# Kernel optimization log

Measured on AMD Instinct MI355X. Metric: run time of the kernel, lower is better.

The kernel has to match this reference:

```python
import jax, jax.numpy as jnp
import numpy as np

N_RAYS = 32768
HID = 64
MARCH_ITERS = 64
EPS = 1e-4
NEAR = 0.0
FAR = 1.0
T_FAR = 1.0
TPUT_B = 64
JITTER = 1.0 / TPUT_B  # fixed stand-in for random.random() * (2 / batch_size)


def _init_linear(key, fan_in, fan_out):
    kw, kb = jax.random.split(key)
    lim = 1.0 / np.sqrt(fan_in)
    W = jax.random.uniform(kw, (fan_in, fan_out), jnp.float32, -lim, lim)
    b = jax.random.uniform(kb, (fan_out,), jnp.float32, -lim, lim)
    return W, b


def setup_inputs() -> dict:
    key = jax.random.key(0)
    ks = jax.random.split(key, 6)
    rays = jax.random.normal(ks[0], (N_RAYS, 6), jnp.float32)
    W0, b0 = _init_linear(ks[1], 3, HID)
    W1, b1 = _init_linear(ks[2], HID, HID)
    W2, b2 = _init_linear(ks[3], HID, 1)
    Wr0, br0 = _init_linear(ks[4], 6, HID)
    Wr1, br1 = _init_linear(ks[5], HID, 3)
    return dict(rays=rays, W0=W0, b0=b0, W1=W1, b1=b1, W2=W2, b2=b2,
                Wr0=Wr0, br0=br0, Wr1=Wr1, br1=br1)


def _sdf(p, W0, b0, W1, b1, W2, b2):
    # p: [N, 3] -> signed distance [N, 1]
    h = jax.nn.relu(p @ W0 + b0)
    h = jax.nn.relu(h @ W1 + b1)
    return h @ W2 + b2


def _refl(p, d, Wr0, br0, Wr1, br1):
    # p, d: [N, 3] -> RGB [N, 3]
    h = jax.nn.relu(jnp.concatenate([p, d], axis=-1) @ Wr0 + br0)
    return jax.nn.sigmoid(h @ Wr1 + br1)


def reference(rays, W0, b0, W1, b1, W2, b2, Wr0, br0, Wr1, br1):
    r_o, r_d = rays[..., :3], rays[..., 3:]
    sdf = lambda p: _sdf(p, W0, b0, W1, b1, W2, b2)

    # --- sphere march (64 fixed iterations; early-exit break is a no-op
    # once all rays hit, since hit rays stop updating) ---
    hits0 = jnp.zeros(r_o.shape[:-1] + (1,), jnp.bool_)
    dist0 = jnp.full(r_o.shape[:-1] + (1,), NEAR, jnp.float32)

    def march(carry, _):
        hits, cd = carry
        d = sdf(r_o + r_d * cd)  # [N, 1]
        hits = hits | ((d < EPS) & (cd >= NEAR) & (cd <= FAR))
        cd = jnp.where(~hits, cd + d, cd)
        return (hits, cd), None

    (hit, t), _ = jax.lax.scan(march, (hits0, dist0), None, length=MARCH_ITERS)
    pts = r_o + r_d * t

    rgb = _refl(pts, r_d, Wr0, br0, Wr1, br1)
    rgb = jnp.where(hit, rgb, 0.0)  # out[~hit] = 0

    # --- throughput (index search under no_grad in the original) ---
    max_t = T_FAR + JITTER
    step = max_t / TPUT_B
    sg = jax.lax.stop_gradient
    sdf_ng = lambda p: _sdf(p, sg(W0), sg(b0), sg(W1), sg(b1), sg(W2), sg(b2))
    r_o_ng, r_d_ng = sg(r_o), sg(r_d)

    curr_min0 = sdf_ng(r_o_ng)[..., 0]          # [N]
    idxs0 = jnp.zeros_like(curr_min0, jnp.int32)

    def tloop(carry, i):
        cm, idxs = carry
        t_i = step * (i + 1).astype(jnp.float32)
        sd = sdf_ng(r_o_ng + t_i * r_d_ng)[..., 0]
        idxs = jnp.where(sd < cm, i + 1, idxs)
        return (jnp.minimum(cm, sd), idxs), None

    (_, idxs), _ = jax.lax.scan(tloop, (curr_min0, idxs0),
                                jnp.arange(TPUT_B, dtype=jnp.int32))

    best_pos = r_o + idxs[..., None].astype(jnp.float32) * step * r_d  # [N, 3]
    tput = sdf(best_pos)  # [N, 1], differentiable (outside no_grad in torch)

    return jnp.concatenate([rgb, tput], axis=-1)  # [N, 4]
```

## Files before the change

kernel.cpp:

```cpp
#include <hip/hip_runtime.h>
#include <math.h>

#define NRAYS        32768
#define MARCH_ITERS  64
#define EPS_         1e-4f
#define STEP_        ((1.0f + 1.0f/64.0f) / 64.0f)

typedef __attribute__((ext_vector_type(8)))  short    short8;
typedef __attribute__((ext_vector_type(4)))  float    float4v;
typedef __attribute__((ext_vector_type(4)))  unsigned uint4v;

__device__ __forceinline__ short8 mk_frag(unsigned p0, unsigned p1,
                                          unsigned p2, unsigned p3) {
    uint4v v = {p0, p1, p2, p3};
    return __builtin_bit_cast(short8, v);
}

__device__ __forceinline__ unsigned packbf(unsigned a, unsigned b) {
    return __builtin_amdgcn_perm(b, a, 0x07060302u);
}

struct Split3 { unsigned h, m, l; };
__device__ __forceinline__ Split3 split3(float x) {
    unsigned xu = __float_as_uint(x);
    float xh = __uint_as_float(xu & 0xFFFF0000u);
    float r  = x - xh;
    unsigned ru = __float_as_uint(r);
    float xm = __uint_as_float(ru & 0xFFFF0000u);
    float r2 = r - xm;
    return { xu, ru, __float_as_uint(r2) };
}

struct Split2 { unsigned h, r; };
__device__ __forceinline__ Split2 split2(float x) {
    unsigned xu = __float_as_uint(x);
    float xh = __uint_as_float(xu & 0xFFFF0000u);
    float rr = x - xh;
    return { xu, __float_as_uint(rr) };
}

__global__ __launch_bounds__(64)
__attribute__((amdgpu_waves_per_eu(2, 2)))
void sdf_w7_k(
    const float* __restrict__ rays,
    const float* __restrict__ W0,  const float* __restrict__ b0,
    const float* __restrict__ W1,  const float* __restrict__ b1,
    const float* __restrict__ W2,  const float* __restrict__ b2,
    const float* __restrict__ Wr0, const float* __restrict__ br0,
    const float* __restrict__ Wr1, const float* __restrict__ br1,
    float* __restrict__ out)
{
    const int lane = threadIdx.x;
    const int kind = blockIdx.x & 1;
    const int quad = lane >> 4;
    const int m    = lane & 15;
    const int rayBase = (blockIdx.x >> 1) * 16;

    const float* rp = rays + (rayBase + m) * 6;
    const float ox = rp[0], oy = rp[1], oz = rp[2];
    const float dx = rp[3], dy = rp[4], dz = rp[5];

    short8 A1[4];
    {
        const float* wbase = (quad == 0) ? W0 : (quad == 1) ? (W0 + 64)
                           : (quad == 2) ? (W0 + 128) : b0;
        #pragma unroll
        for (int t = 0; t < 4; ++t) {
            int j = 32 * (t >> 1) + 8 * (m >> 2) + 4 * (t & 1) + (m & 3);
            Split3 s = split3(wbase[j]);
            unsigned hh = packbf(s.h, s.h);
            unsigned hm = packbf(s.h, s.m);
            unsigned ml = packbf(s.m, s.l);
            unsigned l0 = packbf(s.l, 0u);
            bool is3 = (quad == 3);
            A1[t] = mk_frag(is3 ? hm : hh, is3 ? l0 : hm, is3 ? 0u : ml, 0u);
        }
    }

    float4v b1v[4], w2v[4];
    #pragma unroll
    for (int t = 0; t < 4; ++t) {
        int base = 16 * t + 4 * quad;
        b1v[t] = (float4v){b1[base], b1[base + 1], b1[base + 2], b1[base + 3]};
        w2v[t] = (float4v){W2[base], W2[base + 1], W2[base + 2], W2[base + 3]};
    }
    const float b2s = b2[0];
    const float4v z4 = {0.f, 0.f, 0.f, 0.f};

    auto buildB1 = [&](float px, float py, float pz) -> short8 {
        float c = (quad == 0) ? px : (quad == 1) ? py : pz;
        Split3 s = split3(c);
        unsigned d0 = packbf(s.h, s.m);
        unsigned d1 = packbf(s.l, s.h);
        unsigned d2 = packbf(s.m, s.h);
        if (quad == 3) { d0 = 0x3F803F80u; d1 = 0x00003F80u; d2 = 0u; }
        return mk_frag(d0, d1, d2, 0u);
    };

    auto front = [&](float px, float py, float pz, short8* BH, short8* BM) {
        short8 B1 = buildB1(px, py, pz);
        float4v C1[4];
        #pragma unroll
        for (int t = 0; t < 4; ++t)
            C1[t] = __builtin_amdgcn_mfma_f32_16x16x32_bf16(A1[t], B1, z4, 0, 0, 0);
        unsigned PH[4][2], PM[4][2];
        #pragma unroll
        for (int t = 0; t < 4; ++t) {
            float v0 = fmaxf(C1[t][0], 0.f), v1 = fmaxf(C1[t][1], 0.f);
            float v2 = fmaxf(C1[t][2], 0.f), v3 = fmaxf(C1[t][3], 0.f);
            unsigned u0 = __float_as_uint(v0), u1 = __float_as_uint(v1);
            unsigned u2 = __float_as_uint(v2), u3 = __float_as_uint(v3);
            PH[t][0] = packbf(u0, u1); PH[t][1] = packbf(u2, u3);
            float r0 = v0 - __uint_as_float(u0 & 0xFFFF0000u);
            float r1 = v1 - __uint_as_float(u1 & 0xFFFF0000u);
            float r2 = v2 - __uint_as_float(u2 & 0xFFFF0000u);
            float r3 = v3 - __uint_as_float(u3 & 0xFFFF0000u);
            PM[t][0] = packbf(__float_as_uint(r0), __float_as_uint(r1));
            PM[t][1] = packbf(__float_as_uint(r2), __float_as_uint(r3));
        }
        #pragma unroll
        for (int h = 0; h < 2; ++h) {
            BH[h] = mk_frag(PH[2 * h][0], PH[2 * h][1],
                            PH[2 * h + 1][0], PH[2 * h + 1][1]);
            BM[h] = mk_frag(PM[2 * h][0], PM[2 * h][1],
                            PM[2 * h + 1][0], PM[2 * h + 1][1]);
        }
    };

    auto l3 = [&](const float4v* C2) -> float {
        float q0 = 0.f, q1 = 0.f, q2 = 0.f, q3 = 0.f;
        #pragma unroll
        for (int t = 0; t < 4; ++t) {
            q0 = fmaf(fmaxf(C2[t][0], 0.f), w2v[t][0], q0);
            q1 = fmaf(fmaxf(C2[t][1], 0.f), w2v[t][1], q1);
            q2 = fmaf(fmaxf(C2[t][2], 0.f), w2v[t][2], q2);
            q3 = fmaf(fmaxf(C2[t][3], 0.f), w2v[t][3], q3);
        }
        float part = (q0 + q1) + (q2 + q3);
        part += __shfl_xor(part, 16, 64);
        part += __shfl_xor(part, 32, 64);
        return b2s + part;
    };

    if (kind == 0) {
        short8 A2h[2][4], A2m[2][4];
        #pragma unroll
        for (int h = 0; h < 2; ++h)
            #pragma unroll
            for (int t = 0; t < 4; ++t) {
                unsigned pm[4], ph[4];
                #pragma unroll
                for (int jp = 0; jp < 4; ++jp) {
                    int k0 = 32 * h + quad * 8 + 2 * jp;
                    int j2 = 16 * t + m;
                    Split2 a = split2(W1[k0 * 64 + j2]);
                    Split2 b = split2(W1[(k0 + 1) * 64 + j2]);
                    pm[jp] = packbf(a.r, b.r);
                    ph[jp] = packbf(a.h, b.h);
                }
                A2m[h][t] = mk_frag(pm[0], pm[1], pm[2], pm[3]);
                A2h[h][t] = mk_frag(ph[0], ph[1], ph[2], ph[3]);
            }

        bool  hit = false;
        float cd  = 0.f;
        #pragma unroll 1
        for (int it = 0; it < MARCH_ITERS; ++it) {
            if (__all(hit)) break;
            short8 BH[2], BM[2];
            front(fmaf(dx, cd, ox), fmaf(dy, cd, oy), fmaf(dz, cd, oz), BH, BM);
            float4v C2[4];
            #pragma unroll
            for (int t = 0; t < 4; ++t) C2[t] = b1v[t];
            #pragma unroll
            for (int h = 0; h < 2; ++h)
                #pragma unroll
                for (int t = 0; t < 4; ++t)
                    C2[t] = __builtin_amdgcn_mfma_f32_16x16x32_bf16(
                        A2m[h][t], BH[h], C2[t], 0, 0, 0);
            #pragma unroll
            for (int h = 0; h < 2; ++h)
                #pragma unroll
                for (int t = 0; t < 4; ++t)
                    C2[t] = __builtin_amdgcn_mfma_f32_16x16x32_bf16(
                        A2h[h][t], BM[h], C2[t], 0, 0, 0);
            #pragma unroll
            for (int h = 0; h < 2; ++h)
                #pragma unroll
                for (int t = 0; t < 4; ++t)
                    C2[t] = __builtin_amdgcn_mfma_f32_16x16x32_bf16(
                        A2h[h][t], BH[h], C2[t], 0, 0, 0);
            float dm = l3(C2);
            bool c = (dm < EPS_) && (cd >= 0.f) && (cd <= 1.f);
            hit = hit || c;
            if (!hit) cd += dm;
        }

        const float px = fmaf(dx, cd, ox), py = fmaf(dy, cd, oy), pz = fmaf(dz, cd, oz);
        float r0 = 0.f, r1 = 0.f, r2 = 0.f;
        #pragma unroll 4
        for (int jj = 0; jj < 16; ++jj) {
            int j = quad * 16 + jj;
            float a = fmaf(px, Wr0[j],
                      fmaf(py, Wr0[64 + j],
                      fmaf(pz, Wr0[128 + j],
                      fmaf(dx, Wr0[192 + j],
                      fmaf(dy, Wr0[256 + j],
                      fmaf(dz, Wr0[320 + j], br0[j]))))));
            a = fmaxf(a, 0.f);
            r0 = fmaf(a, Wr1[j * 3 + 0], r0);
            r1 = fmaf(a, Wr1[j * 3 + 1], r1);
            r2 = fmaf(a, Wr1[j * 3 + 2], r2);
        }
        r0 += __shfl_xor(r0, 16, 64); r0 += __shfl_xor(r0, 32, 64);
        r1 += __shfl_xor(r1, 16, 64); r1 += __shfl_xor(r1, 32, 64);
        r2 += __shfl_xor(r2, 16, 64); r2 += __shfl_xor(r2, 32, 64);
        r0 = 1.f / (1.f + expf(-(r0 + br1[0])));
        r1 = 1.f / (1.f + expf(-(r1 + br1[1])));
        r2 = 1.f / (1.f + expf(-(r2 + br1[2])));
        if (!hit) { r0 = 0.f; r1 = 0.f; r2 = 0.f; }
        if (lane < 16) {
            float* op = out + (rayBase + lane) * 4;
            op[0] = r0; op[1] = r1; op[2] = r2;
        }
    } else {
        short8 A2h[2][4];
        #pragma unroll
        for (int h = 0; h < 2; ++h)
            #pragma unroll
            for (int t = 0; t < 4; ++t) {
                unsigned ph[4];
                #pragma unroll
                for (int jp = 0; jp < 4; ++jp) {
                    int k0 = 32 * h + quad * 8 + 2 * jp;
                    int j2 = 16 * t + m;
                    ph[jp] = packbf(__float_as_uint(W1[k0 * 64 + j2]),
                                    __float_as_uint(W1[(k0 + 1) * 64 + j2]));
                }
                A2h[h][t] = mk_frag(ph[0], ph[1], ph[2], ph[3]);
            }

        float cm = 3.4e38f;
        #pragma unroll 1
        for (int i = 0; i <= 64; ++i) {
            float ti = STEP_ * (float)i;
            short8 BH[2], BM[2];
            front(fmaf(dx, ti, ox), fmaf(dy, ti, oy), fmaf(dz, ti, oz), BH, BM);
            float4v C2[4];
            #pragma unroll
            for (int t = 0; t < 4; ++t) C2[t] = b1v[t];
            #pragma unroll
            for (int h = 0; h < 2; ++h)
                #pragma unroll
                for (int t = 0; t < 4; ++t)
                    C2[t] = __builtin_amdgcn_mfma_f32_16x16x32_bf16(
                        A2h[h][t], BM[h], C2[t], 0, 0, 0);
            #pragma unroll
            for (int h = 0; h < 2; ++h)
                #pragma unroll
                for (int t = 0; t < 4; ++t)
                    C2[t] = __builtin_amdgcn_mfma_f32_16x16x32_bf16(
                        A2h[h][t], BH[h], C2[t], 0, 0, 0);
            float dt = l3(C2);
            cm = fminf(cm, dt);
        }
        if (lane < 16)
            out[(rayBase + lane) * 4 + 3] = cm;
    }
}

extern "C" void kernel_launch(void* const* d_in, const int* in_sizes, int n_in,
                              void* d_out, int out_size, void* d_ws, size_t ws_size,
                              hipStream_t stream) {
    const float* rays = (const float*)d_in[0];
    const float* W0   = (const float*)d_in[1];
    const float* b0   = (const float*)d_in[2];
    const float* W1   = (const float*)d_in[3];
    const float* b1   = (const float*)d_in[4];
    const float* W2   = (const float*)d_in[5];
    const float* b2   = (const float*)d_in[6];
    const float* Wr0  = (const float*)d_in[7];
    const float* br0  = (const float*)d_in[8];
    const float* Wr1  = (const float*)d_in[9];
    const float* br1  = (const float*)d_in[10];
    float* out = (float*)d_out;

    hipLaunchKernelGGL(sdf_w7_k, dim3((NRAYS / 16) * 2), dim3(64), 0, stream,
                       rays, W0, b0, W1, b1, W2, b2, Wr0, br0, Wr1, br1, out);
}
```

Baseline: 188.2 us.

## Process two 16-ray tiles per wave to interleave independent MFMA chains

```diff
diff --git a/kernel.cpp b/kernel.cpp
--- a/kernel.cpp
+++ b/kernel.cpp
@@ -41,7 +41,7 @@
 
 __global__ __launch_bounds__(64)
 __attribute__((amdgpu_waves_per_eu(2, 2)))
-void sdf_w7_k(
+void sdf_w8_k(
     const float* __restrict__ rays,
     const float* __restrict__ W0,  const float* __restrict__ b0,
     const float* __restrict__ W1,  const float* __restrict__ b1,
@@ -54,11 +54,15 @@
     const int kind = blockIdx.x & 1;
     const int quad = lane >> 4;
     const int m    = lane & 15;
-    const int rayBase = (blockIdx.x >> 1) * 16;
-
-    const float* rp = rays + (rayBase + m) * 6;
-    const float ox = rp[0], oy = rp[1], oz = rp[2];
-    const float dx = rp[3], dy = rp[4], dz = rp[5];
+    const int rayBase = (blockIdx.x >> 1) * 32;
+
+    float oxA[2], oyA[2], ozA[2], dxA[2], dyA[2], dzA[2];
+    #pragma unroll
+    for (int c = 0; c < 2; ++c) {
+        const float* rp = rays + (rayBase + 16 * c + m) * 6;
+        oxA[c] = rp[0]; oyA[c] = rp[1]; ozA[c] = rp[2];
+        dxA[c] = rp[3]; dyA[c] = rp[4]; dzA[c] = rp[5];
+    }
 
     short8 A1[4];
     {
@@ -162,66 +166,86 @@
                 A2h[h][t] = mk_frag(ph[0], ph[1], ph[2], ph[3]);
             }
 
-        bool  hit = false;
-        float cd  = 0.f;
+        bool  hit[2] = {false, false};
+        float cd[2]  = {0.f, 0.f};
         #pragma unroll 1
         for (int it = 0; it < MARCH_ITERS; ++it) {
-            if (__all(hit)) break;
-            short8 BH[2], BM[2];
-            front(fmaf(dx, cd, ox), fmaf(dy, cd, oy), fmaf(dz, cd, oz), BH, BM);
-            float4v C2[4];
-            #pragma unroll
-            for (int t = 0; t < 4; ++t) C2[t] = b1v[t];
-            #pragma unroll
-            for (int h = 0; h < 2; ++h)
-                #pragma unroll
-                for (int t = 0; t < 4; ++t)
-                    C2[t] = __builtin_amdgcn_mfma_f32_16x16x32_bf16(
-                        A2m[h][t], BH[h], C2[t], 0, 0, 0);
-            #pragma unroll
-            for (int h = 0; h < 2; ++h)
-                #pragma unroll
-                for (int t = 0; t < 4; ++t)
-                    C2[t] = __builtin_amdgcn_mfma_f32_16x16x32_bf16(
-                        A2h[h][t], BM[h], C2[t], 0, 0, 0);
-            #pragma unroll
-            for (int h = 0; h < 2; ++h)
-                #pragma unroll
-                for (int t = 0; t < 4; ++t)
-                    C2[t] = __builtin_amdgcn_mfma_f32_16x16x32_bf16(
-                        A2h[h][t], BH[h], C2[t], 0, 0, 0);
-            float dm = l3(C2);
-            bool c = (dm < EPS_) && (cd >= 0.f) && (cd <= 1.f);
-            hit = hit || c;
-            if (!hit) cd += dm;
-        }
-
-        const float px = fmaf(dx, cd, ox), py = fmaf(dy, cd, oy), pz = fmaf(dz, cd, oz);
-        float r0 = 0.f, r1 = 0.f, r2 = 0.f;
-        #pragma unroll 4
-        for (int jj = 0; jj < 16; ++jj) {
-            int j = quad * 16 + jj;
-            float a = fmaf(px, Wr0[j],
-                      fmaf(py, Wr0[64 + j],
-                      fmaf(pz, Wr0[128 + j],
-                      fmaf(dx, Wr0[192 + j],
-                      fmaf(dy, Wr0[256 + j],
-                      fmaf(dz, Wr0[320 + j], br0[j]))))));
-            a = fmaxf(a, 0.f);
-            r0 = fmaf(a, Wr1[j * 3 + 0], r0);
-            r1 = fmaf(a, Wr1[j * 3 + 1], r1);
-            r2 = fmaf(a, Wr1[j * 3 + 2], r2);
-        }
-        r0 += __shfl_xor(r0, 16, 64); r0 += __shfl_xor(r0, 32, 64);
-        r1 += __shfl_xor(r1, 16, 64); r1 += __shfl_xor(r1, 32, 64);
-        r2 += __shfl_xor(r2, 16, 64); r2 += __shfl_xor(r2, 32, 64);
-        r0 = 1.f / (1.f + expf(-(r0 + br1[0])));
-        r1 = 1.f / (1.f + expf(-(r1 + br1[1])));
-        r2 = 1.f / (1.f + expf(-(r2 + br1[2])));
-        if (!hit) { r0 = 0.f; r1 = 0.f; r2 = 0.f; }
-        if (lane < 16) {
-            float* op = out + (rayBase + lane) * 4;
-            op[0] = r0; op[1] = r1; op[2] = r2;
+            if (__all(hit[0] & hit[1])) break;
+            short8 BH[2][2], BM[2][2];
+            #pragma unroll
+            for (int c = 0; c < 2; ++c)
+                front(fmaf(dxA[c], cd[c], oxA[c]),
+                      fmaf(dyA[c], cd[c], oyA[c]),
+                      fmaf(dzA[c], cd[c], ozA[c]), BH[c], BM[c]);
+            float4v C2[2][4];
+            #pragma unroll
+            for (int c = 0; c < 2; ++c)
+                #pragma unroll
+                for (int t = 0; t < 4; ++t) C2[c][t] = b1v[t];
+            #pragma unroll
+            for (int h = 0; h < 2; ++h)
+                #pragma unroll
+                for (int c = 0; c < 2; ++c)
+                    #pragma unroll
+                    for (int t = 0; t < 4; ++t)
+                        C2[c][t] = __builtin_amdgcn_mfma_f32_16x16x32_bf16(
+                            A2m[h][t], BH[c][h], C2[c][t], 0, 0, 0);
+            #pragma unroll
+            for (int h = 0; h < 2; ++h)
+                #pragma unroll
+                for (int c = 0; c < 2; ++c)
+                    #pragma unroll
+                    for (int t = 0; t < 4; ++t)
+                        C2[c][t] = __builtin_amdgcn_mfma_f32_16x16x32_bf16(
+                            A2h[h][t], BM[c][h], C2[c][t], 0, 0, 0);
+            #pragma unroll
+            for (int h = 0; h < 2; ++h)
+                #pragma unroll
+                for (int c = 0; c < 2; ++c)
+                    #pragma unroll
+                    for (int t = 0; t < 4; ++t)
+                        C2[c][t] = __builtin_amdgcn_mfma_f32_16x16x32_bf16(
+                            A2h[h][t], BH[c][h], C2[c][t], 0, 0, 0);
+            #pragma unroll
+            for (int c = 0; c < 2; ++c) {
+                float dm = l3(C2[c]);
+                bool cc = (dm < EPS_) && (cd[c] >= 0.f) && (cd[c] <= 1.f);
+                hit[c] = hit[c] || cc;
+                if (!hit[c]) cd[c] += dm;
+            }
+        }
+
+        #pragma unroll
+        for (int c = 0; c < 2; ++c) {
+            const float px = fmaf(dxA[c], cd[c], oxA[c]);
+            const float py = fmaf(dyA[c], cd[c], oyA[c]);
+            const float pz = fmaf(dzA[c], cd[c], ozA[c]);
+            float r0 = 0.f, r1 = 0.f, r2 = 0.f;
+            #pragma unroll 4
+            for (int jj = 0; jj < 16; ++jj) {
+                int j = quad * 16 + jj;
+                float a = fmaf(px, Wr0[j],
+                          fmaf(py, Wr0[64 + j],
+                          fmaf(pz, Wr0[128 + j],
+                          fmaf(dxA[c], Wr0[192 + j],
+                          fmaf(dyA[c], Wr0[256 + j],
+                          fmaf(dzA[c], Wr0[320 + j], br0[j]))))));
+                a = fmaxf(a, 0.f);
+                r0 = fmaf(a, Wr1[j * 3 + 0], r0);
+                r1 = fmaf(a, Wr1[j * 3 + 1], r1);
+                r2 = fmaf(a, Wr1[j * 3 + 2], r2);
+            }
+            r0 += __shfl_xor(r0, 16, 64); r0 += __shfl_xor(r0, 32, 64);
+            r1 += __shfl_xor(r1, 16, 64); r1 += __shfl_xor(r1, 32, 64);
+            r2 += __shfl_xor(r2, 16, 64); r2 += __shfl_xor(r2, 32, 64);
+            r0 = 1.f / (1.f + expf(-(r0 + br1[0])));
+            r1 = 1.f / (1.f + expf(-(r1 + br1[1])));
+            r2 = 1.f / (1.f + expf(-(r2 + br1[2])));
+            if (!hit[c]) { r0 = 0.f; r1 = 0.f; r2 = 0.f; }
+            if (lane < 16) {
+                float* op = out + (rayBase + 16 * c + lane) * 4;
+                op[0] = r0; op[1] = r1; op[2] = r2;
+            }
         }
     } else {
         short8 A2h[2][4];
@@ -240,32 +264,45 @@
                 A2h[h][t] = mk_frag(ph[0], ph[1], ph[2], ph[3]);
             }
 
-        float cm = 3.4e38f;
+        float cm[2] = {3.4e38f, 3.4e38f};
         #pragma unroll 1
         for (int i = 0; i <= 64; ++i) {
             float ti = STEP_ * (float)i;
-            short8 BH[2], BM[2];
-            front(fmaf(dx, ti, ox), fmaf(dy, ti, oy), fmaf(dz, ti, oz), BH, BM);
-            float4v C2[4];
-            #pragma unroll
-            for (int t = 0; t < 4; ++t) C2[t] = b1v[t];
-            #pragma unroll
-            for (int h = 0; h < 2; ++h)
-                #pragma unroll
-                for (int t = 0; t < 4; ++t)
-                    C2[t] = __builtin_amdgcn_mfma_f32_16x16x32_bf16(
-                        A2h[h][t], BM[h], C2[t], 0, 0, 0);
-            #pragma unroll
-            for (int h = 0; h < 2; ++h)
-                #pragma unroll
-                for (int t = 0; t < 4; ++t)
-                    C2[t] = __builtin_amdgcn_mfma_f32_16x16x32_bf16(
-                        A2h[h][t], BH[h], C2[t], 0, 0, 0);
-            float dt = l3(C2);
-            cm = fminf(cm, dt);
-        }
-        if (lane < 16)
-            out[(rayBase + lane) * 4 + 3] = cm;
+            short8 BH[2][2], BM[2][2];
+            #pragma unroll
+            for (int c = 0; c < 2; ++c)
+                front(fmaf(dxA[c], ti, oxA[c]),
+                      fmaf(dyA[c], ti, oyA[c]),
+                      fmaf(dzA[c], ti, ozA[c]), BH[c], BM[c]);
+            float4v C2[2][4];
+            #pragma unroll
+            for (int c = 0; c < 2; ++c)
+                #pragma unroll
+                for (int t = 0; t < 4; ++t) C2[c][t] = b1v[t];
+            #pragma unroll
+            for (int h = 0; h < 2; ++h)
+                #pragma unroll
+                for (int c = 0; c < 2; ++c)
+                    #pragma unroll
+                    for (int t = 0; t < 4; ++t)
+                        C2[c][t] = __builtin_amdgcn_mfma_f32_16x16x32_bf16(
+                            A2h[h][t], BM[c][h], C2[c][t], 0, 0, 0);
+            #pragma unroll
+            for (int h = 0; h < 2; ++h)
+                #pragma unroll
+                for (int c = 0; c < 2; ++c)
+                    #pragma unroll
+                    for (int t = 0; t < 4; ++t)
+                        C2[c][t] = __builtin_amdgcn_mfma_f32_16x16x32_bf16(
+                            A2h[h][t], BH[c][h], C2[c][t], 0, 0, 0);
+            #pragma unroll
+            for (int c = 0; c < 2; ++c)
+                cm[c] = fminf(cm[c], l3(C2[c]));
+        }
+        if (lane < 16) {
+            out[(rayBase + lane) * 4 + 3]      = cm[0];
+            out[(rayBase + 16 + lane) * 4 + 3] = cm[1];
+        }
     }
 }
 
@@ -285,6 +322,6 @@
     const float* br1  = (const float*)d_in[10];
     float* out = (float*)d_out;
 
-    hipLaunchKernelGGL(sdf_w7_k, dim3((NRAYS / 16) * 2), dim3(64), 0, stream,
+    hipLaunchKernelGGL(sdf_w8_k, dim3((NRAYS / 32) * 2), dim3(64), 0, stream,
                        rays, W0, b0, W1, b1, W2, b2, Wr0, br0, Wr1, br1, out);
 }
```

Result: no change. 187.7 us (-0.2%).
